# Kernel optimization log

Measured on AMD Instinct MI355X. Metric: run time of the kernel, lower is better.

## Reference

```python
import jax, jax.numpy as jnp
import numpy as np

EPS = 1e-5

def _inorm(t):
    # InstanceNorm2d, affine=False: normalize each (B,C) plane over H,W
    m = t.mean((2, 3), keepdims=True)
    v = t.var((2, 3), keepdims=True)
    return (t - m) * jax.lax.rsqrt(v + EPS)

def _conv(x, w, b):
    y = jax.lax.conv_general_dilated(x, w, (1, 1), 'SAME',
        dimension_numbers=('NCHW', 'OIHW', 'NCHW'))
    return y + b[None, :, None, None]

def _ss2d(xh, in_proj_w, conv_w, conv_b, x_proj_w, dt_w, dt_b, A_logs, Ds,
          out_norm_g, out_norm_b, out_proj_w):
    # xh: (B,H,W,C) -> (B,H,W,C). VMamba-style 4-direction selective scan.
    B, H, W, C = xh.shape
    Di = in_proj_w.shape[0] // 2
    n = A_logs.shape[-1]
    R = dt_w.shape[-1]
    L = H * W
    xz = xh @ in_proj_w.T                      # (B,H,W,2*Di)
    xin, z = xz[..., :Di], xz[..., Di:]
    xc = xin.transpose(0, 3, 1, 2)             # (B,Di,H,W)
    xc = jax.lax.conv_general_dilated(xc, conv_w, (1, 1), 'SAME',
        feature_group_count=Di, dimension_numbers=('NCHW', 'OIHW', 'NCHW'))
    xc = jax.nn.silu(xc + conv_b[None, :, None, None])
    x1 = xc.reshape(B, Di, L)                  # row-major scan
    x2 = xc.transpose(0, 1, 3, 2).reshape(B, Di, L)  # col-major scan
    xs = jnp.stack([x1, x2, x1[..., ::-1], x2[..., ::-1]], axis=1)  # (B,4,Di,L)
    x_dbl = jnp.einsum('bkdl,kcd->bkcl', xs, x_proj_w)
    dts = jnp.einsum('bkrl,kdr->bkdl', x_dbl[:, :, :R], dt_w)
    Bs, Cs = x_dbl[:, :, R:R + n], x_dbl[:, :, R + n:]
    delta = jax.nn.softplus(dts + dt_b[None, :, :, None])
    A = -jnp.exp(A_logs)                       # (4,Di,n)
    scan_in = (jnp.moveaxis(xs, -1, 0), jnp.moveaxis(delta, -1, 0),
               jnp.moveaxis(Bs, -1, 0), jnp.moveaxis(Cs, -1, 0))
    def step(h, inp):
        u, d, b, c = inp                       # u,d:(B,4,Di)  b,c:(B,4,n)
        h = jnp.exp(d[..., None] * A) * h + (d * u)[..., None] * b[:, :, None, :]
        return h, (h * c[:, :, None, :]).sum(-1)
    h0 = jnp.zeros((B, 4, Di, n), xh.dtype)
    _, ys = jax.lax.scan(step, h0, scan_in)    # ys: (L,B,4,Di)
    out_y = jnp.moveaxis(ys, 0, -1) + Ds[None, :, :, None] * xs  # (B,4,Di,L)
    def _wh(t):
        return t.reshape(B, Di, W, H).transpose(0, 1, 3, 2).reshape(B, Di, L)
    y = out_y[:, 0] + out_y[:, 2, :, ::-1] + _wh(out_y[:, 1]) + _wh(out_y[:, 3, :, ::-1])
    y = y.transpose(0, 2, 1).reshape(B, H, W, Di)
    mu = y.mean(-1, keepdims=True)
    v = y.var(-1, keepdims=True)
    y = (y - mu) * jax.lax.rsqrt(v + EPS) * out_norm_g + out_norm_b
    return (y * jax.nn.silu(z)) @ out_proj_w.T

def setup_inputs():
    key = jax.random.key(0)
    ks = jax.random.split(key, 16)
    B, C, H, W = 4, 96, 64, 64
    Di, n, R, K, SQ, CC = 192, 8, 6, 4, 16, 16
    f = jnp.float32
    nrm = lambda k, s: 0.02 * jax.random.normal(k, s, dtype=f)
    inp = {}
    inp['x'] = jax.random.normal(ks[0], (B, C, H, W), dtype=f)
    inp['dz'] = jax.random.uniform(ks[1], (B, 1, H, W), dtype=f)
    inp['in_proj_w'] = nrm(ks[2], (2 * Di, C))
    inp['conv_w'] = nrm(ks[3], (Di, 1, 3, 3))
    inp['conv_b'] = jnp.zeros((Di,), f)
    inp['x_proj_w'] = nrm(ks[4], (K, R + 2 * n, Di))
    inp['dt_w'] = nrm(ks[5], (K, Di, R))
    inp['dt_b'] = 0.01 * jnp.ones((K, Di), f)
    inp['A_logs'] = jnp.log(jnp.tile(jnp.arange(1, n + 1, dtype=f)[None, None, :], (K, Di, 1)))
    inp['Ds'] = jnp.ones((K, Di), f)
    inp['out_norm_g'] = jnp.ones((Di,), f)
    inp['out_norm_b'] = jnp.zeros((Di,), f)
    inp['out_proj_w'] = nrm(ks[6], (C, Di))
    inp['ln_g'] = jnp.ones((C,), f)
    inp['ln_b'] = jnp.zeros((C,), f)
    inp['skip_ss2d'] = jnp.ones((C,), f)
    inp['cca_w1'] = nrm(ks[7], (SQ, C))
    inp['cca_b1'] = jnp.zeros((SQ,), f)
    inp['cca_w2'] = nrm(ks[8], (C, SQ))
    inp['cca_b2'] = jnp.zeros((C,), f)
    inp['bnc_w1'] = nrm(ks[9], (CC, C, 1, 1))
    inp['bnc_b1'] = jnp.zeros((CC,), f)
    inp['bnc_w2'] = nrm(ks[10], (CC, CC, 3, 3))
    inp['bnc_b2'] = jnp.zeros((CC,), f)
    inp['bnc_w3'] = nrm(ks[11], (C, CC, 1, 1))
    inp['bnc_b3'] = jnp.zeros((C,), f)
    return inp

def reference(x, dz, in_proj_w, conv_w, conv_b, x_proj_w, dt_w, dt_b, A_logs, Ds,
              out_norm_g, out_norm_b, out_proj_w, ln_g, ln_b, skip_ss2d,
              cca_w1, cca_b1, cca_w2, cca_b2,
              bnc_w1, bnc_b1, bnc_w2, bnc_b2, bnc_w3, bnc_b3):
    SKIP_CCA, SKIP_BNC = 0.4, 1.0
    # 1) channel cross-attention block (dz-guided SE), residual w/ skip 0.4
    xn = _inorm(x)
    pooled = (xn * dz).sum((2, 3)) / (dz.sum((2, 3)) + 1e-6)  # (B,C)
    s = jax.nn.sigmoid(jax.nn.relu(pooled @ cca_w1.T + cca_b1) @ cca_w2.T + cca_b2)
    x = xn * s[:, :, None, None] + SKIP_CCA * x
    # 2) SS2D block in NHWC, residual w/ learned per-channel skip weight
    xh = x.transpose(0, 2, 3, 1)
    mu = xh.mean(-1, keepdims=True)
    v = xh.var(-1, keepdims=True)
    xln = (xh - mu) * jax.lax.rsqrt(v + EPS) * ln_g + ln_b
    y = _ss2d(xln, in_proj_w, conv_w, conv_b, x_proj_w, dt_w, dt_b, A_logs, Ds,
              out_norm_g, out_norm_b, out_proj_w)
    x = (y + skip_ss2d * xh).transpose(0, 3, 1, 2)
    # 3) bottleneck conv block, residual w/ skip 1.0
    xn = _inorm(x)
    h = jax.nn.relu(_conv(xn, bnc_w1, bnc_b1))
    h = jax.nn.relu(_conv(h, bnc_w2, bnc_b2))
    h = _conv(h, bnc_w3, bnc_b3)
    return h + SKIP_BNC * x
```

## Files before the change

### kernel.cpp

```cpp
#include <hip/hip_runtime.h>
#include <hip/hip_bf16.h>
#include <math.h>

constexpr int TOT_IN = 1685008;

constexpr size_t F_x    = 64;
constexpr size_t F_dz   = F_x + 1572864;
constexpr size_t F_ipw  = F_dz + 16384;
constexpr size_t F_convw= F_ipw + 36864;
constexpr size_t F_convb= F_convw + 1728;
constexpr size_t F_xpw  = F_convb + 192;
constexpr size_t F_dtw  = F_xpw + 16896;
constexpr size_t F_dtb  = F_dtw + 4608;
constexpr size_t F_alog = F_dtb + 768;
constexpr size_t F_Dsv  = F_alog + 6144;
constexpr size_t F_ong  = F_Dsv + 768;
constexpr size_t F_onb  = F_ong + 192;
constexpr size_t F_opw  = F_onb + 192;
constexpr size_t F_lng  = F_opw + 18432;
constexpr size_t F_lnb  = F_lng + 96;
constexpr size_t F_skip = F_lnb + 96;
constexpr size_t F_cw1  = F_skip + 96;
constexpr size_t F_cb1  = F_cw1 + 1536;
constexpr size_t F_cw2  = F_cb1 + 16;
constexpr size_t F_cb2  = F_cw2 + 1536;
constexpr size_t F_bw1  = F_cb2 + 96;
constexpr size_t F_bb1  = F_bw1 + 1536;
constexpr size_t F_bw2  = F_bb1 + 16;
constexpr size_t F_bb2  = F_bw2 + 2304;
constexpr size_t F_bw3  = F_bb2 + 16;
constexpr size_t F_bb3  = F_bw3 + 1536;
constexpr size_t F_stat = 1685504;
constexpr size_t F_mean1= F_stat;
constexpr size_t F_rstd1= F_stat + 384;
constexpr size_t F_wsum = F_stat + 768;
constexpr size_t F_sca  = F_stat + 1216;
constexpr size_t F_mean2= F_stat + 1664;
constexpr size_t F_rstd2= F_stat + 2048;
constexpr size_t F_xcca = 1689600;
constexpr size_t F_xln  = F_xcca + 1572864;
constexpr size_t F_xin  = F_xln  + 1572864;
constexpr size_t F_z    = F_xin  + 3145728;
constexpr size_t F_xct  = F_z    + 3145728;
constexpr size_t F_xdbl = F_xct  + 3145728;
constexpr size_t F_old1 = F_xdbl + 1572864;
constexpr size_t F_xccaT= F_old1 + 3145728;
constexpr size_t F_yc   = F_xccaT+ 1572864;
constexpr size_t F_tb   = F_yc   + 3145728;
constexpr size_t F_x2   = F_tb   + 3145728;
constexpr size_t F_h1   = F_x2   + 1572864;
constexpr size_t F_h2   = F_h1   + 262144;
constexpr size_t F_xpwt = F_h2   + 262144;
constexpr size_t F_ipwt = F_xpwt + 18432;
constexpr size_t F_opwt = F_ipwt + 36864;
constexpr size_t F_cwt  = F_opwt + 18432;
constexpr size_t F_hend = F_xin;
constexpr size_t F_apr  = F_tb;
constexpr size_t F_hcar = F_old1;

__constant__ int y4off[16] = {
  3262464, 4048896, 4835328, 5621760, 6408192, 7194624,
  18991104, 19777536,
  20563968, 21350400, 22136832, 22923264,
  23709696, 24496128, 25282560, 26068992};

__constant__ int g_off[27] = {
  0,1572864,1589248,1626112,1627840,1628032,1644928,1649536,1650304,1656448,
  1657216,1657408,1657600,1676032,1676128,1676224,1676320,1677856,1677872,1679408,
  1679504,1681040,1681056,1683360,1683376,1684912,1685008};

struct Ptrs26 { const void* p[26]; };

static __device__ __forceinline__ float sigmoidf_(float x){ return 1.f/(1.f+__expf(-x)); }
static __device__ __forceinline__ float siluf_(float x){ return x*sigmoidf_(x); }
static __device__ __forceinline__ float softplusf_(float x){ return x>15.f ? x : log1pf(__expf(x)); }
static __device__ __forceinline__ int mapk_(int k,int l){
  switch(k){
    case 0: return l;
    case 1: return ((l&63)<<6)|(l>>6);
    case 2: return 4095-l;
    default:{ int l2=4095-l; return ((l2&63)<<6)|(l2>>6); }
  }
}

__global__ void k_convert(Ptrs26 ps, float* __restrict__ F){
  int bf = (((const unsigned int*)ps.p[9])[0] == 0x3F803F80u) ? 1 : 0;
  int stride = gridDim.x*blockDim.x;
  for (int idx = blockIdx.x*blockDim.x+threadIdx.x; idx < TOT_IN; idx += stride){
    int lo = 0, hi = 26;
    while (hi - lo > 1){ int mid = (lo+hi)>>1; if (idx >= g_off[mid]) lo = mid; else hi = mid; }
    int s = lo;
    int loc = idx - g_off[s];
    float v;
    if (bf) v = __bfloat162float(((const __hip_bfloat16*)ps.p[s])[loc]);
    else    v = ((const float*)ps.p[s])[loc];
    F[64 + idx] = v;
  }
}

__global__ void k_wtrans(float* __restrict__ F){
  int idx = blockIdx.x*256 + threadIdx.x;
  if (idx < 18432){
    int c = idx % 24; int d = (idx/24) % 192; int k = idx/(24*192);
    F[F_xpwt + idx] = (c < 22) ? F[F_xpw + (size_t)(k*22 + c)*192 + d] : 0.f;
  } else if (idx < 18432 + 36864){
    int i = idx - 18432;
    int j = i % 384, c = i / 384;
    F[F_ipwt + i] = F[F_ipw + (size_t)j*96 + c];
  } else if (idx < 18432 + 36864 + 18432){
    int i = idx - 18432 - 36864;
    int c = i % 96, d = i / 96;
    F[F_opwt + i] = F[F_opw + (size_t)c*192 + d];
  } else if (idx < 18432 + 36864 + 18432 + 1728){
    int i = idx - 18432 - 36864 - 18432;
    int d = i % 192, tap = i / 192;
    F[F_cwt + i] = F[F_convw + (size_t)d*9 + tap];
  }
}

__global__ void k_inorm1(float* __restrict__ F){
  int bc = blockIdx.x; int b = bc/96;
  const float* xp  = F + F_x  + (size_t)bc*4096;
  const float* dzp = F + F_dz + (size_t)b*4096;
  float s=0.f, s2=0.f, sw=0.f;
  for (int l=threadIdx.x; l<4096; l+=256){ float v=xp[l]; s+=v; s2+=v*v; sw+=v*dzp[l]; }
  for (int m=32;m;m>>=1){ s+=__shfl_xor(s,m); s2+=__shfl_xor(s2,m); sw+=__shfl_xor(sw,m); }
  __shared__ float red[12];
  int wid = threadIdx.x>>6;
  if ((threadIdx.x&63)==0){ red[wid]=s; red[4+wid]=s2; red[8+wid]=sw; }
  __syncthreads();
  if (threadIdx.x==0){
    s = red[0]+red[1]+red[2]+red[3];
    s2= red[4]+red[5]+red[6]+red[7];
    sw= red[8]+red[9]+red[10]+red[11];
    float mean = s*(1.f/4096.f);
    float var  = s2*(1.f/4096.f) - mean*mean;
    F[F_mean1+bc]=mean; F[F_rstd1+bc]=rsqrtf(var+1e-5f); F[F_wsum+bc]=sw;
  }
}

__global__ void k_cca(float* __restrict__ F){
  __shared__ float ps[96], hid[16], red[2];
  int b = blockIdx.x, t = threadIdx.x;
  const float* dzp = F + F_dz + (size_t)b*4096;
  float s=0.f;
  for (int l=t; l<4096; l+=128) s += dzp[l];
  for (int m=32;m;m>>=1) s += __shfl_xor(s,m);
  if ((t&63)==0) red[t>>6] = s;
  __syncthreads();
  float dzs = red[0]+red[1];
  if (t<96){
    int bc = b*96+t;
    ps[t] = F[F_rstd1+bc]*(F[F_wsum+bc]-F[F_mean1+bc]*dzs)/(dzs+1e-6f);
  }
  __syncthreads();
  if (t<16){
    float a = F[F_cb1+t];
    for (int c=0;c<96;c++) a += ps[c]*F[F_cw1+t*96+c];
    hid[t] = fmaxf(a,0.f);
  }
  __syncthreads();
  if (t<96){
    float a = F[F_cb2+t];
    for (int j=0;j<16;j++) a += hid[j]*F[F_cw2+t*16+j];
    F[F_sca+b*96+t] = sigmoidf_(a);
  }
}

__global__ __launch_bounds__(256) void k_ccat(float* __restrict__ F){
  __shared__ float T[96*33];
  __shared__ float mns[32], rss[32];
  int b = blockIdx.x >> 7; int l0 = (blockIdx.x & 127)*32;
  for (int i = threadIdx.x; i < 3072; i += 256){
    int l = i & 31, c = i >> 5;
    int bc = b*96 + c;
    float v = F[F_x + (size_t)bc*4096 + l0 + l];
    float xv = (v - F[F_mean1+bc])*F[F_rstd1+bc]*F[F_sca+bc] + 0.4f*v;
    F[F_xcca + (size_t)bc*4096 + l0 + l] = xv;
    T[c*33 + l] = xv;
  }
  __syncthreads();
  {
    int l = threadIdx.x >> 3, p = threadIdx.x & 7;
    float s=0.f, s2=0.f;
    for (int c=p; c<96; c+=8){ float v = T[c*33 + l]; s+=v; s2+=v*v; }
    for (int m=4;m;m>>=1){ s += __shfl_xor(s,m); s2 += __shfl_xor(s2,m); }
    if (p==0){
      float mean = s*(1.f/96.f);
      mns[l] = mean;
      rss[l] = rsqrtf(s2*(1.f/96.f) - mean*mean + 1e-5f);
    }
  }
  __syncthreads();
  for (int i = threadIdx.x; i < 3072; i += 256){
    int c = i % 96, l = i / 96;
    float xv = T[c*33 + l];
    F[F_xccaT + ((size_t)(b*4096 + l0 + l))*96 + c] =
        (xv - mns[l])*rss[l]*F[F_lng+c] + F[F_lnb+c];
  }
}

__global__ __launch_bounds__(256) void k_gemm1(
    const float* __restrict__ xln, const float* __restrict__ wt1,
    float* __restrict__ xin, float* __restrict__ z)
{
  __shared__ float As[96*68];
  __shared__ float Ws[96*68];
  int lt = blockIdx.x & 255, jb = blockIdx.x >> 8;
  int l0 = lt*64, j0 = jb*64;
  for (int i = threadIdx.x; i < 6144; i += 256){
    int li = i / 96, c = i - (i/96)*96;
    As[c*68 + li] = xln[((size_t)(l0+li))*96 + c];
  }
  for (int i = threadIdx.x; i < 6144; i += 256){
    int c = i >> 6, jj = i & 63;
    Ws[c*68 + jj] = wt1[(size_t)c*384 + j0 + jj];
  }
  __syncthreads();
  int li0 = (threadIdx.x & 15)*4, jj0 = (threadIdx.x >> 4)*4;
  float acc[4][4] = {};
  #pragma unroll 4
  for (int c = 0; c < 96; c++){
    float4 a = *(const float4*)(As + c*68 + li0);
    float4 w = *(const float4*)(Ws + c*68 + jj0);
    float ar[4] = {a.x, a.y, a.z, a.w};
    float wr[4] = {w.x, w.y, w.z, w.w};
    #pragma unroll
    for (int r=0;r<4;r++)
      #pragma unroll
      for (int q=0;q<4;q++) acc[r][q] += ar[r]*wr[q];
  }
  float* base = (j0 < 192) ? xin : z;
  int joff = (j0 < 192) ? (j0 + jj0) : (j0 - 192 + jj0);
  #pragma unroll
  for (int r=0;r<4;r++){
    *(float4*)&base[(size_t)(l0+li0+r)*192 + joff] =
        make_float4(acc[r][0], acc[r][1], acc[r][2], acc[r][3]);
  }
}

__global__ void k_dwconv(const float* __restrict__ xin, const float* __restrict__ cwt,
                         const float* __restrict__ cb, float* __restrict__ xct){
  int idx = blockIdx.x*256 + threadIdx.x;
  if (idx >= 786432) return;
  int d4 = idx % 48; int bl = idx / 48; int l = bl & 4095; int b = bl >> 12;
  int h = l >> 6, w = l & 63;
  const float4* xp = (const float4*)(xin + (size_t)b*4096*192);
  const float4* wp = (const float4*)cwt;
  float4 bias = ((const float4*)cb)[d4];
  float ax=bias.x, ay=bias.y, az=bias.z, aw=bias.w;
  #pragma unroll
  for (int ky=0; ky<3; ky++){
    int hh = h + ky - 1; if ((unsigned)hh > 63u) continue;
    #pragma unroll
    for (int kx=0; kx<3; kx++){
      int ww = w + kx - 1; if ((unsigned)ww > 63u) continue;
      float4 xv = xp[(size_t)(hh*64+ww)*48 + d4];
      float4 wv = wp[(ky*3+kx)*48 + d4];
      ax += xv.x*wv.x; ay += xv.y*wv.y; az += xv.z*wv.z; aw += xv.w*wv.w;
    }
  }
  float4 o;
  o.x = ax*sigmoidf_(ax); o.y = ay*sigmoidf_(ay);
  o.z = az*sigmoidf_(az); o.w = aw*sigmoidf_(aw);
  ((float4*)xct)[idx] = o;
}

__global__ __launch_bounds__(256) void k_xdbl(
    const float* __restrict__ xct, const float* __restrict__ wt,
    float* __restrict__ xdbl)
{
  int lb = blockIdx.x & 15; int bk = blockIdx.x >> 4;
  int b = bk >> 2, k = bk & 3;
  int l = lb*256 + threadIdx.x;
  int sp = mapk_(k, l);
  const float4* rp = (const float4*)(xct + ((size_t)b*4096 + sp)*192);
  const float* wk = wt + (size_t)k*192*24;
  float acc[24];
  #pragma unroll
  for (int c=0;c<24;c++) acc[c]=0.f;
  #pragma unroll 2
  for (int d4=0; d4<48; d4++){
    float4 av = rp[d4];
    #pragma unroll
    for (int j=0;j<4;j++){
      float ad = (j==0)?av.x:(j==1)?av.y:(j==2)?av.z:av.w;
      const float* wd = wk + (d4*4+j)*24;
      #pragma unroll
      for (int c=0;c<22;c++) acc[c] += ad * wd[c];
    }
  }
  acc[22]=0.f; acc[23]=0.f;
  float4* op = (float4*)(xdbl + ((size_t)bk*4096 + l)*24);
  #pragma unroll
  for (int q=0;q<6;q++) op[q] = make_float4(acc[q*4],acc[q*4+1],acc[q*4+2],acc[q*4+3]);
}

__global__ __launch_bounds__(192) void k_scan1(
    const float* __restrict__ xdbl, const float* __restrict__ xct,
    const float* __restrict__ alogs, const float* __restrict__ dtws,
    const float* __restrict__ dtbs,
    float* __restrict__ hend, float* __restrict__ apr)
{
  int chunk = blockIdx.x & 127; int bk = blockIdx.x >> 7;
  int b = bk >> 2, k = bk & 3; int d = threadIdx.x;
  const float* alog = alogs + (size_t)(k*192+d)*8;
  float A_[8], hh[8], ap[8];
  #pragma unroll
  for (int i=0;i<8;i++){ A_[i] = -__expf(alog[i]); hh[i]=0.f; ap[i]=1.f; }
  bool structured = fabsf(A_[0] + 1.f) < 1e-4f;
  #pragma unroll
  for (int i=1;i<8;i++) structured = structured && (fabsf(A_[i] - (float)(i+1)*A_[0]) <= 1e-4f*fabsf(A_[i]));
  float dtw_[6];
  #pragma unroll
  for (int r=0;r<6;r++) dtw_[r] = dtws[(size_t)(k*192+d)*6 + r];
  float dtb_ = dtbs[k*192 + d];
  const float* xB = xdbl + ((size_t)bk*4096 + chunk*32)*24;
  const float* xc = xct + (size_t)b*4096*192 + d;
  if (structured){
    #pragma unroll 4
    for (int s=0;s<32;s++){
      const float* xl = xB + s*24;
      float dt = dtb_;
      #pragma unroll
      for (int r=0;r<6;r++) dt += xl[r]*dtw_[r];
      int sp = mapk_(k, chunk*32+s);
      float u = xc[(size_t)sp*192];
      float t = __expf(dt);
      float a1 = __builtin_amdgcn_rcpf(1.f + t);
      float delta = (dt > 15.f) ? dt : __logf(1.f + t);
      float du = delta*u;
      float a = a1;
      #pragma unroll
      for (int i=0;i<8;i++){
        hh[i] = a*hh[i] + du*xl[6+i];
        ap[i] *= a;
        a *= a1;
      }
    }
  } else {
    for (int s=0;s<32;s++){
      const float* xl = xB + s*24;
      float dt = dtb_;
      #pragma unroll
      for (int r=0;r<6;r++) dt += xl[r]*dtw_[r];
      int sp = mapk_(k, chunk*32+s);
      float u = xc[(size_t)sp*192];
      float delta = softplusf_(dt);
      float du = delta*u;
      #pragma unroll
      for (int i=0;i<8;i++){
        float a = __expf(delta*A_[i]);
        hh[i] = a*hh[i] + du*xl[6+i];
        ap[i] *= a;
      }
    }
  }
  size_t base = ((size_t)(bk<<7) + chunk)*1536 + d*8;
  #pragma unroll
  for (int i=0;i<8;i++){ hend[base+i]=hh[i]; apr[base+i]=ap[i]; }
}

__global__ void k_carry(const float* __restrict__ hend, const float* __restrict__ apr,
                        float* __restrict__ hcar){
  int t = blockIdx.x*256 + threadIdx.x;
  if (t >= 16*1536) return;
  int di8 = t % 1536; int bk = t / 1536;
  float carry = 0.f;
  for (int c=0;c<128;c++){
    size_t idx = ((size_t)(bk<<7) + c)*1536 + di8;
    hcar[idx] = carry;
    carry = apr[idx]*carry + hend[idx];
  }
}

__global__ __launch_bounds__(192) void k_scan2(
    const float* __restrict__ xdbl, const float* __restrict__ xct,
    const float* __restrict__ alogs, const float* __restrict__ dtws,
    const float* __restrict__ dtbs, const float* __restrict__ Dsv,
    const float* __restrict__ hcar, float* __restrict__ yout)
{
  int chunk = blockIdx.x & 127; int bk = blockIdx.x >> 7;
  int b = bk >> 2, k = bk & 3; int d = threadIdx.x;
  const float* alog = alogs + (size_t)(k*192+d)*8;
  float A_[8], hh[8];
  size_t cb = ((size_t)(bk<<7) + chunk)*1536 + d*8;
  #pragma unroll
  for (int i=0;i<8;i++){ A_[i] = -__expf(alog[i]); hh[i] = hcar[cb+i]; }
  bool structured = fabsf(A_[0] + 1.f) < 1e-4f;
  #pragma unroll
  for (int i=1;i<8;i++) structured = structured && (fabsf(A_[i] - (float)(i+1)*A_[0]) <= 1e-4f*fabsf(A_[i]));
  float dtw_[6];
  #pragma unroll
  for (int r=0;r<6;r++) dtw_[r] = dtws[(size_t)(k*192+d)*6 + r];
  float dtb_ = dtbs[k*192 + d];
  float Dsc  = Dsv[k*192 + d];
  const float* xB = xdbl + ((size_t)bk*4096 + chunk*32)*24;
  const float* xc = xct + (size_t)b*4096*192 + d;
  float* yo = yout + (size_t)y4off[bk] + ((size_t)(chunk*32))*192 + d;
  if (structured){
    #pragma unroll 4
    for (int s=0;s<32;s++){
      const float* xl = xB + s*24;
      float dt = dtb_;
      #pragma unroll
      for (int r=0;r<6;r++) dt += xl[r]*dtw_[r];
      int sp = mapk_(k, chunk*32+s);
      float u = xc[(size_t)sp*192];
      float t = __expf(dt);
      float a1 = __builtin_amdgcn_rcpf(1.f + t);
      float delta = (dt > 15.f) ? dt : __logf(1.f + t);
      float du = delta*u;
      float a = a1, y = 0.f;
      #pragma unroll
      for (int i=0;i<8;i++){
        hh[i] = a*hh[i] + du*xl[6+i];
        y += hh[i]*xl[14+i];
        a *= a1;
      }
      yo[(size_t)s*192] = y + Dsc*u;
    }
  } else {
    for (int s=0;s<32;s++){
      const float* xl = xB + s*24;
      float dt = dtb_;
      #pragma unroll
      for (int r=0;r<6;r++) dt += xl[r]*dtw_[r];
      int sp = mapk_(k, chunk*32+s);
      float u = xc[(size_t)sp*192];
      float delta = softplusf_(dt);
      float du = delta*u;
      float y = 0.f;
      #pragma unroll
      for (int i=0;i<8;i++){
        float a = __expf(delta*A_[i]);
        hh[i] = a*hh[i] + du*xl[6+i];
        y += hh[i]*xl[14+i];
      }
      yo[(size_t)s*192] = y + Dsc*u;
    }
  }
}

__global__ void k_tnorm(float* __restrict__ F){
  int wid = threadIdx.x >> 6, lane = threadIdx.x & 63;
  int p = blockIdx.x*4 + wid;
  int b = p >> 12, sp = p & 4095;
  int l1 = ((sp&63)<<6)|(sp>>6);
  const float* y0 = F + (size_t)y4off[b*4+0] + (size_t)sp*192;
  const float* y1 = F + (size_t)y4off[b*4+1] + (size_t)l1*192;
  const float* y2 = F + (size_t)y4off[b*4+2] + (size_t)(4095-sp)*192;
  const float* y3 = F + (size_t)y4off[b*4+3] + (size_t)(4095-l1)*192;
  float v[3]; float s=0.f, s2=0.f;
  #pragma unroll
  for (int j=0;j<3;j++){
    int dd = j*64+lane;
    v[j] = y0[dd] + y1[dd] + y2[dd] + y3[dd];
    s += v[j]; s2 += v[j]*v[j];
  }
  for (int m=32;m;m>>=1){ s+=__shfl_xor(s,m); s2+=__shfl_xor(s2,m); }
  float mean = s*(1.f/192.f);
  float rstd = rsqrtf(s2*(1.f/192.f) - mean*mean + 1e-5f);
  size_t base = (size_t)p*192;
  #pragma unroll
  for (int j=0;j<3;j++){
    int dd = j*64+lane;
    float zv = F[F_z + base + dd];
    float t = (v[j]-mean)*rstd*F[F_ong+dd] + F[F_onb+dd];
    F[F_xct + base + dd] = t * siluf_(zv);
  }
}

__global__ __launch_bounds__(128) void k_gemm2(
    const float* __restrict__ tb, const float* __restrict__ wt2,
    const float* __restrict__ skip, const float* __restrict__ xcca,
    float* __restrict__ x2)
{
  int lb = blockIdx.x & 127; int cbk = blockIdx.x >> 7;
  int t = lb*128 + threadIdx.x;
  int b = t >> 12, l = t & 4095;
  const float4* rp = (const float4*)(tb + (size_t)t*192);
  const float* wbase = wt2 + cbk*12;
  float acc[12];
  #pragma unroll
  for (int c=0;c<12;c++) acc[c]=0.f;
  #pragma unroll 2
  for (int d4=0; d4<48; d4++){
    float4 av = rp[d4];
    #pragma unroll
    for (int dd=0; dd<4; dd++){
      float ad = (dd==0)?av.x:(dd==1)?av.y:(dd==2)?av.z:av.w;
      const float* wr = wbase + (size_t)(d4*4+dd)*96;
      #pragma unroll
      for (int c=0;c<12;c++) acc[c] += ad * wr[c];
    }
  }
  #pragma unroll
  for (int c=0;c<12;c++){
    int cg = cbk*12 + c;
    size_t o = ((size_t)(b*96+cg))*4096 + l;
    x2[o] = acc[c] + skip[cg]*xcca[o];
  }
}

__global__ void k_inorm2(float* __restrict__ F){
  int bc = blockIdx.x;
  const float* xp = F + F_x2 + (size_t)bc*4096;
  float s=0.f, s2=0.f;
  for (int l=threadIdx.x; l<4096; l+=256){ float v=xp[l]; s+=v; s2+=v*v; }
  for (int m=32;m;m>>=1){ s+=__shfl_xor(s,m); s2+=__shfl_xor(s2,m); }
  __shared__ float red[8];
  int wid = threadIdx.x>>6;
  if ((threadIdx.x&63)==0){ red[wid]=s; red[4+wid]=s2; }
  __syncthreads();
  if (threadIdx.x==0){
    s = red[0]+red[1]+red[2]+red[3];
    s2= red[4]+red[5]+red[6]+red[7];
    float mean = s*(1.f/4096.f);
    float var  = s2*(1.f/4096.f) - mean*mean;
    F[F_mean2+bc]=mean; F[F_rstd2+bc]=rsqrtf(var+1e-5f);
  }
}

__global__ void k_bnc1(float* __restrict__ F){
  int idx = blockIdx.x*256 + threadIdx.x;
  if (idx >= 4*16*4096) return;
  int l = idx & 4095; int bj = idx >> 12; int j = bj % 16; int b = bj / 16;
  float acc = F[F_bb1 + j];
  const float* wp = F + F_bw1 + j*96;
  for (int c=0;c<96;c++){
    int bc = b*96+c;
    float xn = (F[F_x2 + (size_t)bc*4096 + l] - F[F_mean2+bc])*F[F_rstd2+bc];
    acc += xn*wp[c];
  }
  F[F_h1+idx] = fmaxf(acc, 0.f);
}

__global__ void k_bnc2(float* __restrict__ F){
  int idx = blockIdx.x*256 + threadIdx.x;
  if (idx >= 4*16*4096) return;
  int l = idx & 4095; int bj = idx >> 12; int j = bj % 16; int b = bj / 16;
  int h = l >> 6, w = l & 63;
  float acc = F[F_bb2 + j];
  const float* h1p = F + F_h1 + (size_t)b*16*4096;
  const float* wp  = F + F_bw2 + j*16*9;
  for (int jp=0; jp<16; jp++){
    #pragma unroll
    for (int ky=0; ky<3; ky++){
      int hh = h + ky - 1; if (hh < 0 || hh > 63) continue;
      #pragma unroll
      for (int kx=0; kx<3; kx++){
        int ww = w + kx - 1; if (ww < 0 || ww > 63) continue;
        acc += h1p[(size_t)jp*4096 + hh*64+ww] * wp[jp*9 + ky*3 + kx];
      }
    }
  }
  F[F_h2+idx] = fmaxf(acc, 0.f);
}

__global__ void k_bnc3(float* __restrict__ F, void* __restrict__ out, const unsigned int* __restrict__ ds){
  int idx = blockIdx.x*256 + threadIdx.x;
  if (idx >= 1572864) return;
  int l = idx & 4095; int bc = idx >> 12; int c = bc % 96; int b = bc / 96;
  float acc = F[F_bb3 + c];
  const float* h2p = F + F_h2 + (size_t)b*16*4096 + l;
  const float* wp  = F + F_bw3 + c*16;
  #pragma unroll
  for (int j=0;j<16;j++) acc += h2p[(size_t)j*4096]*wp[j];
  float res = acc + F[F_x2+idx];
  if (ds[0]==0x3F803F80u) ((__hip_bfloat16*)out)[idx] = __float2bfloat16(res);
  else                    ((float*)out)[idx] = res;
}

extern "C" void kernel_launch(void* const* d_in, const int* in_sizes, int n_in,
                              void* d_out, int out_size, void* d_ws, size_t ws_size,
                              hipStream_t stream) {
  (void)in_sizes; (void)n_in; (void)out_size; (void)ws_size;
  float* F = (float*)d_ws;

  Ptrs26 ps;
  for (int i=0;i<26;i++) ps.p[i] = d_in[i];

  k_convert<<<2048, 256, 0, stream>>>(ps, F);
  k_wtrans<<<296, 256, 0, stream>>>(F);

  k_inorm1<<<384, 256, 0, stream>>>(F);
  k_cca   <<<4,   128, 0, stream>>>(F);
  k_ccat  <<<512, 256, 0, stream>>>(F);
  k_gemm1 <<<1536,256, 0, stream>>>(F+F_xccaT, F+F_ipwt, F+F_xin, F+F_z);
  k_dwconv<<<3072,256, 0, stream>>>(F+F_xin, F+F_cwt, F+F_convb, F+F_xct);
  k_xdbl  <<<256, 256, 0, stream>>>(F+F_xct, F+F_xpwt, F+F_xdbl);
  k_scan1 <<<2048,192, 0, stream>>>(F+F_xdbl, F+F_xct, F+F_alog, F+F_dtw, F+F_dtb,
                                    F+F_hend, F+F_apr);
  k_carry <<<96,  256, 0, stream>>>(F+F_hend, F+F_apr, F+F_hcar);
  k_scan2 <<<2048,192, 0, stream>>>(F+F_xdbl, F+F_xct, F+F_alog, F+F_dtw, F+F_dtb,
                                    F+F_Dsv, F+F_hcar, F);
  k_tnorm <<<4096,256, 0, stream>>>(F);
  k_gemm2 <<<1024,128, 0, stream>>>(F+F_xct, F+F_opwt, F+F_skip, F+F_xcca, F+F_x2);
  k_inorm2<<<384, 256, 0, stream>>>(F);
  k_bnc1  <<<1024,256, 0, stream>>>(F);
  k_bnc2  <<<1024,256, 0, stream>>>(F);
  k_bnc3  <<<6144,256, 0, stream>>>(F, d_out, (const unsigned int*)d_in[9]);
}
```

Baseline: 368.6 us.

## Fuse bottleneck conv stages into one tiled kernel; split xdbl columns; coalesce carry layout

Three separate bottleneck kernels (1x1 conv, 3x3 conv, 1x1 conv plus residual) are merged into one kernel. Each block handles an 8x8 spatial tile with a halo and keeps the normalized input, h1 and h2 in shared memory, so the h1/h2 global round trips and two launches go away. The halo 1x1 conv is recomputed per tile, and the fused kernel launches only 256 blocks with a large shared-memory footprint, which can limit occupancy. Separately, k_xdbl splits its 22 output columns across two blocks to double parallelism and cut registers. The scan carry buffers are also re-laid out as state-major with d innermost, so k_scan1, k_carry and k_scan2 access them coalesced.

```diff
diff --git a/kernel.cpp b/kernel.cpp
--- a/kernel.cpp
+++ b/kernel.cpp
@@ -270,15 +270,15 @@
     const float* __restrict__ xct, const float* __restrict__ wt,
     float* __restrict__ xdbl)
 {
-  int lb = blockIdx.x & 15; int bk = blockIdx.x >> 4;
+  int cc = blockIdx.x & 1; int lb = (blockIdx.x >> 1) & 15; int bk = blockIdx.x >> 5;
   int b = bk >> 2, k = bk & 3;
   int l = lb*256 + threadIdx.x;
   int sp = mapk_(k, l);
   const float4* rp = (const float4*)(xct + ((size_t)b*4096 + sp)*192);
-  const float* wk = wt + (size_t)k*192*24;
-  float acc[24];
-  #pragma unroll
-  for (int c=0;c<24;c++) acc[c]=0.f;
+  const float* wk = wt + (size_t)k*192*24 + cc*12;
+  float acc[12];
+  #pragma unroll
+  for (int c=0;c<12;c++) acc[c]=0.f;
   #pragma unroll 2
   for (int d4=0; d4<48; d4++){
     float4 av = rp[d4];
@@ -287,13 +287,12 @@
       float ad = (j==0)?av.x:(j==1)?av.y:(j==2)?av.z:av.w;
       const float* wd = wk + (d4*4+j)*24;
       #pragma unroll
-      for (int c=0;c<22;c++) acc[c] += ad * wd[c];
-    }
-  }
-  acc[22]=0.f; acc[23]=0.f;
-  float4* op = (float4*)(xdbl + ((size_t)bk*4096 + l)*24);
-  #pragma unroll
-  for (int q=0;q<6;q++) op[q] = make_float4(acc[q*4],acc[q*4+1],acc[q*4+2],acc[q*4+3]);
+      for (int c=0;c<12;c++) acc[c] += ad * wd[c];
+    }
+  }
+  float4* op = (float4*)(xdbl + ((size_t)bk*4096 + l)*24 + cc*12);
+  #pragma unroll
+  for (int q=0;q<3;q++) op[q] = make_float4(acc[q*4],acc[q*4+1],acc[q*4+2],acc[q*4+3]);
 }
 
 __global__ __launch_bounds__(192) void k_scan1(
@@ -356,19 +355,19 @@
       }
     }
   }
-  size_t base = ((size_t)(bk<<7) + chunk)*1536 + d*8;
-  #pragma unroll
-  for (int i=0;i<8;i++){ hend[base+i]=hh[i]; apr[base+i]=ap[i]; }
+  size_t base = ((size_t)(bk*128 + chunk)*8)*192 + d;
+  #pragma unroll
+  for (int i=0;i<8;i++){ hend[base+(size_t)i*192]=hh[i]; apr[base+(size_t)i*192]=ap[i]; }
 }
 
 __global__ void k_carry(const float* __restrict__ hend, const float* __restrict__ apr,
                         float* __restrict__ hcar){
   int t = blockIdx.x*256 + threadIdx.x;
   if (t >= 16*1536) return;
-  int di8 = t % 1536; int bk = t / 1536;
+  int d = t % 192; int i = (t/192) & 7; int bk = t / 1536;
   float carry = 0.f;
   for (int c=0;c<128;c++){
-    size_t idx = ((size_t)(bk<<7) + c)*1536 + di8;
+    size_t idx = ((size_t)(bk*128 + c)*8 + i)*192 + d;
     hcar[idx] = carry;
     carry = apr[idx]*carry + hend[idx];
   }
@@ -384,9 +383,9 @@
   int b = bk >> 2, k = bk & 3; int d = threadIdx.x;
   const float* alog = alogs + (size_t)(k*192+d)*8;
   float A_[8], hh[8];
-  size_t cb = ((size_t)(bk<<7) + chunk)*1536 + d*8;
-  #pragma unroll
-  for (int i=0;i<8;i++){ A_[i] = -__expf(alog[i]); hh[i] = hcar[cb+i]; }
+  size_t cb = ((size_t)(bk*128 + chunk)*8)*192 + d;
+  #pragma unroll
+  for (int i=0;i<8;i++){ A_[i] = -__expf(alog[i]); hh[i] = hcar[cb+(size_t)i*192]; }
   bool structured = fabsf(A_[0] + 1.f) < 1e-4f;
   #pragma unroll
   for (int i=1;i<8;i++) structured = structured && (fabsf(A_[i] - (float)(i+1)*A_[0]) <= 1e-4f*fabsf(A_[i]));
@@ -522,54 +521,65 @@
   }
 }
 
-__global__ void k_bnc1(float* __restrict__ F){
-  int idx = blockIdx.x*256 + threadIdx.x;
-  if (idx >= 4*16*4096) return;
-  int l = idx & 4095; int bj = idx >> 12; int j = bj % 16; int b = bj / 16;
-  float acc = F[F_bb1 + j];
-  const float* wp = F + F_bw1 + j*96;
-  for (int c=0;c<96;c++){
-    int bc = b*96+c;
-    float xn = (F[F_x2 + (size_t)bc*4096 + l] - F[F_mean2+bc])*F[F_rstd2+bc];
-    acc += xn*wp[c];
-  }
-  F[F_h1+idx] = fmaxf(acc, 0.f);
-}
-
-__global__ void k_bnc2(float* __restrict__ F){
-  int idx = blockIdx.x*256 + threadIdx.x;
-  if (idx >= 4*16*4096) return;
-  int l = idx & 4095; int bj = idx >> 12; int j = bj % 16; int b = bj / 16;
-  int h = l >> 6, w = l & 63;
-  float acc = F[F_bb2 + j];
-  const float* h1p = F + F_h1 + (size_t)b*16*4096;
-  const float* wp  = F + F_bw2 + j*16*9;
-  for (int jp=0; jp<16; jp++){
+__global__ __launch_bounds__(256) void k_bncf(float* __restrict__ F, void* __restrict__ out,
+                                              const unsigned int* __restrict__ ds){
+  __shared__ float XN[9600];
+  __shared__ float H1[1600];
+  __shared__ float H2[1024];
+  int b = blockIdx.x >> 6;
+  int tile = blockIdx.x & 63;
+  int h0 = (tile >> 3)*8, w0 = (tile & 7)*8;
+  for (int i = threadIdx.x; i < 9600; i += 256){
+    int c = i / 100, pos = i - (i/100)*100;
+    int gy = h0 + pos/10 - 1, gx = w0 + pos%10 - 1;
+    float v = 0.f;
+    if ((unsigned)gy < 64u && (unsigned)gx < 64u){
+      int bc = b*96 + c;
+      v = (F[F_x2 + (size_t)bc*4096 + gy*64+gx] - F[F_mean2+bc])*F[F_rstd2+bc];
+    }
+    XN[i] = v;
+  }
+  __syncthreads();
+  for (int i = threadIdx.x; i < 1600; i += 256){
+    int j = i / 100, pos = i - (i/100)*100;
+    int gy = h0 + pos/10 - 1, gx = w0 + pos%10 - 1;
+    float acc = 0.f;
+    if ((unsigned)gy < 64u && (unsigned)gx < 64u){
+      acc = F[F_bb1 + j];
+      const float* wp = F + F_bw1 + j*96;
+      for (int c = 0; c < 96; c++) acc += XN[c*100+pos]*wp[c];
+      acc = fmaxf(acc, 0.f);
+    }
+    H1[i] = acc;
+  }
+  __syncthreads();
+  for (int i = threadIdx.x; i < 1024; i += 256){
+    int j = i >> 6, pos = i & 63;
+    int py = pos >> 3, px = pos & 7;
+    float acc = F[F_bb2 + j];
+    for (int jp = 0; jp < 16; jp++){
+      const float* wp = F + F_bw2 + (size_t)j*144 + jp*9;
+      const float* hp = H1 + jp*100 + py*10 + px;
+      acc += hp[0]*wp[0] + hp[1]*wp[1] + hp[2]*wp[2]
+           + hp[10]*wp[3] + hp[11]*wp[4] + hp[12]*wp[5]
+           + hp[20]*wp[6] + hp[21]*wp[7] + hp[22]*wp[8];
+    }
+    H2[i] = fmaxf(acc, 0.f);
+  }
+  __syncthreads();
+  bool bf = (ds[0]==0x3F803F80u);
+  for (int i = threadIdx.x; i < 6144; i += 256){
+    int c = i >> 6, pos = i & 63;
+    int gy = h0 + (pos>>3), gx = w0 + (pos&7);
+    float acc = F[F_bb3 + c];
+    const float* wp = F + F_bw3 + c*16;
     #pragma unroll
-    for (int ky=0; ky<3; ky++){
-      int hh = h + ky - 1; if (hh < 0 || hh > 63) continue;
-      #pragma unroll
-      for (int kx=0; kx<3; kx++){
-        int ww = w + kx - 1; if (ww < 0 || ww > 63) continue;
-        acc += h1p[(size_t)jp*4096 + hh*64+ww] * wp[jp*9 + ky*3 + kx];
-      }
-    }
-  }
-  F[F_h2+idx] = fmaxf(acc, 0.f);
-}
-
-__global__ void k_bnc3(float* __restrict__ F, void* __restrict__ out, const unsigned int* __restrict__ ds){
-  int idx = blockIdx.x*256 + threadIdx.x;
-  if (idx >= 1572864) return;
-  int l = idx & 4095; int bc = idx >> 12; int c = bc % 96; int b = bc / 96;
-  float acc = F[F_bb3 + c];
-  const float* h2p = F + F_h2 + (size_t)b*16*4096 + l;
-  const float* wp  = F + F_bw3 + c*16;
-  #pragma unroll
-  for (int j=0;j<16;j++) acc += h2p[(size_t)j*4096]*wp[j];
-  float res = acc + F[F_x2+idx];
-  if (ds[0]==0x3F803F80u) ((__hip_bfloat16*)out)[idx] = __float2bfloat16(res);
-  else                    ((float*)out)[idx] = res;
+    for (int j=0;j<16;j++) acc += H2[j*64+pos]*wp[j];
+    size_t o = ((size_t)(b*96+c))*4096 + gy*64+gx;
+    float res = acc + F[F_x2+o];
+    if (bf) ((__hip_bfloat16*)out)[o] = __float2bfloat16(res);
+    else    ((float*)out)[o] = res;
+  }
 }
 
 extern "C" void kernel_launch(void* const* d_in, const int* in_sizes, int n_in,
@@ -589,7 +599,7 @@
   k_ccat  <<<512, 256, 0, stream>>>(F);
   k_gemm1 <<<1536,256, 0, stream>>>(F+F_xccaT, F+F_ipwt, F+F_xin, F+F_z);
   k_dwconv<<<3072,256, 0, stream>>>(F+F_xin, F+F_cwt, F+F_convb, F+F_xct);
-  k_xdbl  <<<256, 256, 0, stream>>>(F+F_xct, F+F_xpwt, F+F_xdbl);
+  k_xdbl  <<<512, 256, 0, stream>>>(F+F_xct, F+F_xpwt, F+F_xdbl);
   k_scan1 <<<2048,192, 0, stream>>>(F+F_xdbl, F+F_xct, F+F_alog, F+F_dtw, F+F_dtb,
                                     F+F_hend, F+F_apr);
   k_carry <<<96,  256, 0, stream>>>(F+F_hend, F+F_apr, F+F_hcar);
@@ -598,7 +608,5 @@
   k_tnorm <<<4096,256, 0, stream>>>(F);
   k_gemm2 <<<1024,128, 0, stream>>>(F+F_xct, F+F_opwt, F+F_skip, F+F_xcca, F+F_x2);
   k_inorm2<<<384, 256, 0, stream>>>(F);
-  k_bnc1  <<<1024,256, 0, stream>>>(F);
-  k_bnc2  <<<1024,256, 0, stream>>>(F);
-  k_bnc3  <<<6144,256, 0, stream>>>(F, d_out, (const unsigned int*)d_in[9]);
-}
+  k_bncf  <<<256, 256, 0, stream>>>(F, d_out, (const unsigned int*)d_in[9]);
+}
```

Measured after the change: 356.6 us. -3.2%, faster.
